# Performance work log

Hardware: AMD Instinct MI355X
Metric: run time of the kernel (lower is better)

## Reference

```python
import jax, jax.numpy as jnp
import numpy as np

INPUT_DIM = 1024
UNITS = 1024

def setup_inputs() -> dict:
    key = jax.random.key(0)
    ks = jax.random.split(key, 7)
    B, S = 4, 2048
    x = jax.random.normal(ks[0], (B, S, INPUT_DIM), dtype=jnp.float32)
    # nn.Linear weights stored as [out, in]; biases [out]
    scale = 1.0 / np.sqrt(INPUT_DIM)
    Wq = jax.random.uniform(ks[1], (UNITS, INPUT_DIM), jnp.float32, -scale, scale)
    bq = jax.random.uniform(ks[2], (UNITS,), jnp.float32, -scale, scale)
    Wk = jax.random.uniform(ks[3], (UNITS, INPUT_DIM), jnp.float32, -scale, scale)
    bk = jax.random.uniform(ks[4], (UNITS,), jnp.float32, -scale, scale)
    Wv = jax.random.uniform(ks[5], (UNITS, INPUT_DIM), jnp.float32, -scale, scale)
    bv = jax.random.uniform(ks[6], (UNITS,), jnp.float32, -scale, scale)
    return {"x": x, "Wq": Wq, "bq": bq, "Wk": Wk, "bk": bk, "Wv": Wv, "bv": bv}

def reference(x, Wq, bq, Wk, bk, Wv, bv):
    # Q/K/V projections: [B,S,D] @ [D,U]
    Q = jnp.einsum('bsd,ud->bsu', x, Wq) + bq
    K = jnp.einsum('bsd,ud->bsu', x, Wk) + bk
    V = jnp.einsum('bsd,ud->bsu', x, Wv) + bv
    scores = jnp.einsum('bqu,bku->bqk', Q, K) / jnp.sqrt(jnp.float32(UNITS))
    attn = jax.nn.softmax(scores, axis=-1)
    return jnp.einsum('bqk,bku->bqu', attn, V)
```

## Files before the change

### kernel.cpp

```cpp
#include <hip/hip_runtime.h>
#include <cstdint>
#include <cstddef>


typedef unsigned short ushort_t;
typedef __attribute__((ext_vector_type(8))) short short8;
typedef __attribute__((ext_vector_type(4))) float f32x4;

#define AS1 __attribute__((address_space(1)))
#define AS3 __attribute__((address_space(3)))

__device__ __forceinline__ ushort_t f2bf(float f) {
    unsigned int u = __float_as_uint(f);
    u += 0x7FFFu + ((u >> 16) & 1u);
    return (ushort_t)(u >> 16);
}
__device__ __forceinline__ float bf2f(ushort_t b) {
    return __uint_as_float(((unsigned)b) << 16);
}

__device__ __forceinline__ void async_ld16(const void* g, unsigned lds_off) {
    __builtin_amdgcn_global_load_lds((const AS1 void*)(uintptr_t)g,
                                     (AS3 void*)(uintptr_t)lds_off,
                                     16, 0, 0);
}

template <typename OT, int EPI, int NB, int BK>
__global__ __launch_bounds__(256, 2) void gemm_bt(
    const ushort_t* __restrict__ A, const ushort_t* __restrict__ B0,
    const ushort_t* __restrict__ B1,
    const float* __restrict__ bias0, const float* __restrict__ bias1,
    OT* __restrict__ C0, OT* __restrict__ C1,
    int K, int lda, int ldb, int ldc, float scale,
    long long aOffZ, long long bOffZ, long long cOffZ)
{
    constexpr int P     = BK / 8;
    constexpr int NCALL = BK / 16;
    constexpr int RPC   = 2048 / BK;

    __shared__ __align__(16) ushort_t As[128 * BK];
    __shared__ __align__(16) ushort_t Bs[NB][128 * BK];
    __shared__ float rs[128];

    const int tid  = threadIdx.x;
    const int wave = tid >> 6;
    const int lane = tid & 63;

    A  += (size_t)blockIdx.z * aOffZ;
    B0 += (size_t)blockIdx.z * bOffZ;
    if (NB == 2) B1 += (size_t)blockIdx.z * bOffZ;

    const int m0 = blockIdx.y * 128;
    const int n0 = blockIdx.x * 128;
    const int wm = (wave >> 1) * 64;
    const int wn = (wave & 1) * 64;

    const unsigned ldsA  = (unsigned)(uintptr_t)&As[0];
    const unsigned ldsB0 = (unsigned)(uintptr_t)&Bs[0][0];
    const unsigned ldsB1 = (NB == 2) ? (unsigned)(uintptr_t)&Bs[NB - 1][0] : 0;

    const int srow = wave * (RPC / 4) + lane / P;
    const int cd   = ((lane & (P - 1)) - srow) & (P - 1);
    const ushort_t* gA  = A  + (size_t)(m0 + srow) * lda + cd * 8;
    const ushort_t* gB0 = B0 + (size_t)(n0 + srow) * ldb + cd * 8;
    const ushort_t* gB1 = (NB == 2) ? B1 + (size_t)(n0 + srow) * ldb + cd * 8
                                    : nullptr;
    const unsigned lw = (wave << 10);

    const int frow = lane & 15;
    const int fg   = lane >> 4;

    f32x4 acc[NB][4][4] = {};
    float rsacc[4] = {0.f, 0.f, 0.f, 0.f};

    for (int k0 = 0; k0 < K; k0 += BK) {
        if (k0) __syncthreads();
#pragma unroll
        for (int c = 0; c < NCALL; ++c) {
            const size_t ro = (size_t)c * RPC;
            async_ld16(gA + ro * lda, ldsA + c * 4096 + lw);
            async_ld16(gB0 + ro * ldb, ldsB0 + c * 4096 + lw);
            if (NB == 2) async_ld16(gB1 + ro * ldb, ldsB1 + c * 4096 + lw);
        }
        gA += BK; gB0 += BK; if (NB == 2) gB1 += BK;
        __syncthreads();

#pragma unroll
        for (int t = 0; t < BK / 32; ++t) {
            const int pa = (((t << 2) + fg + frow) & (P - 1)) << 3;
            short8 af[4], bf[4];
#pragma unroll
            for (int i = 0; i < 4; ++i)
                af[i] = *(const short8*)&As[(wm + i * 16 + frow) * BK + pa];
            if (EPI == 4 && wn == 0) {
#pragma unroll
                for (int i = 0; i < 4; ++i)
#pragma unroll
                    for (int e = 0; e < 8; ++e)
                        rsacc[i] += bf2f((ushort_t)af[i][e]);
            }
#pragma unroll
            for (int j = 0; j < 4; ++j)
                bf[j] = *(const short8*)&Bs[0][(wn + j * 16 + frow) * BK + pa];
#pragma unroll
            for (int i = 0; i < 4; ++i)
#pragma unroll
                for (int j = 0; j < 4; ++j)
                    acc[0][i][j] = __builtin_amdgcn_mfma_f32_16x16x32_bf16(
                        af[i], bf[j], acc[0][i][j], 0, 0, 0);
            if (NB == 2) {
#pragma unroll
                for (int j = 0; j < 4; ++j)
                    bf[j] = *(const short8*)&Bs[NB - 1][(wn + j * 16 + frow) * BK + pa];
#pragma unroll
                for (int i = 0; i < 4; ++i)
#pragma unroll
                    for (int j = 0; j < 4; ++j)
                        acc[NB - 1][i][j] = __builtin_amdgcn_mfma_f32_16x16x32_bf16(
                            af[i], bf[j], acc[NB - 1][i][j], 0, 0, 0);
            }
        }
    }

    if (EPI == 4) {
        if (wn == 0) {
#pragma unroll
            for (int i = 0; i < 4; ++i) {
                float s = rsacc[i];
                s += __shfl_xor(s, 16, 64);
                s += __shfl_xor(s, 32, 64);
                rs[wm + i * 16 + frow] = s;
            }
        }
        __syncthreads();
    }

    const int r0 = (lane >> 4) << 2;
    const int c0 = lane & 15;
#pragma unroll
    for (int o = 0; o < NB; ++o) {
        OT* C = (o == 0) ? C0 : C1;
        C += (size_t)blockIdx.z * cOffZ;
        const float* bia = (o == 0) ? bias0 : bias1;
#pragma unroll
        for (int i = 0; i < 4; ++i) {
            float bm[4];
            if (EPI == 2) {
#pragma unroll
                for (int r = 0; r < 4; ++r)
                    bm[r] = bias0[m0 + wm + i * 16 + r0 + r];
            }
            if (EPI == 4) {
#pragma unroll
                for (int r = 0; r < 4; ++r)
                    bm[r] = 1.0f / rs[wm + i * 16 + r0 + r];
            }
#pragma unroll
            for (int j = 0; j < 4; ++j) {
                const int n = n0 + wn + j * 16 + c0;
                const float bn = (EPI == 1) ? bia[n] : 0.f;
#pragma unroll
                for (int r = 0; r < 4; ++r) {
                    const int m = m0 + wm + i * 16 + r0 + r;
                    float v = acc[o][i][j][r] * scale;
                    if (EPI == 1) v += bn;
                    if (EPI == 2) v += bm[r];
                    if (EPI == 3) v = __expf(v);
                    if (EPI == 4) v *= bm[r];
                    if constexpr (sizeof(OT) == 2)
                        C[(size_t)m * ldc + n] = f2bf(v);
                    else
                        C[(size_t)m * ldc + n] = v;
                }
            }
        }
    }
}

__global__ __launch_bounds__(256) void cvt_all(
    const float* __restrict__ x,  const float* __restrict__ wq,
    const float* __restrict__ wk, const float* __restrict__ wv,
    ushort_t* __restrict__ xb,  ushort_t* __restrict__ wqb,
    ushort_t* __restrict__ wkb, ushort_t* __restrict__ wvb)
{
    const int b = blockIdx.x;
    const float* src; ushort_t* dst; size_t base;
    if (b < 4096)      { src = x;  dst = xb;  base = (size_t)b * 2048; }
    else if (b < 4608) { src = wq; dst = wqb; base = (size_t)(b - 4096) * 2048; }
    else if (b < 5120) { src = wk; dst = wkb; base = (size_t)(b - 4608) * 2048; }
    else               { src = wv; dst = wvb; base = (size_t)(b - 5120) * 2048; }
    const size_t i = base + threadIdx.x * 8;
    const f32x4 a = *(const f32x4*)(src + i);
    const f32x4 c = *(const f32x4*)(src + i + 4);
    short8 o;
    o[0] = (short)f2bf(a[0]); o[1] = (short)f2bf(a[1]);
    o[2] = (short)f2bf(a[2]); o[3] = (short)f2bf(a[3]);
    o[4] = (short)f2bf(c[0]); o[5] = (short)f2bf(c[1]);
    o[6] = (short)f2bf(c[2]); o[7] = (short)f2bf(c[3]);
    *(short8*)(dst + i) = o;
}

extern "C" void kernel_launch(void* const* d_in, const int* in_sizes, int n_in,
                              void* d_out, int out_size, void* d_ws, size_t ws_size,
                              hipStream_t stream)
{
    const float* x  = (const float*)d_in[0];
    const float* Wq = (const float*)d_in[1];
    const float* bq = (const float*)d_in[2];
    const float* Wk = (const float*)d_in[3];
    const float* bk = (const float*)d_in[4];
    const float* Wv = (const float*)d_in[5];
    const float* bv = (const float*)d_in[6];
    float* out = (float*)d_out;

    char* ws = (char*)d_ws;
    const size_t MB = 1ull << 20;
    ushort_t* Xb  = (ushort_t*)(ws);
    ushort_t* Wqb = (ushort_t*)(ws + 16 * MB);
    ushort_t* Wkb = (ushort_t*)(ws + 18 * MB);
    ushort_t* Wvb = (ushort_t*)(ws + 20 * MB);
    ushort_t* Qb  = (ushort_t*)(ws + 32 * MB);
    ushort_t* Kb  = (ushort_t*)(ws + 48 * MB);
    ushort_t* Vt  = (ushort_t*)(ws + 64 * MB);
    ushort_t* Sc  = (ushort_t*)(ws);

    cvt_all<<<dim3(5632), dim3(256), 0, stream>>>(
        x, Wq, Wk, Wv, Xb, Wqb, Wkb, Wvb);

    gemm_bt<ushort_t, 1, 2, 64><<<dim3(8, 64, 1), dim3(256), 0, stream>>>(
        Xb, Wqb, Wkb, bq, bk, Qb, Kb, 1024, 1024, 1024, 1024, 1.0f, 0, 0, 0);

    gemm_bt<ushort_t, 2, 1, 64><<<dim3(64, 8, 1), dim3(256), 0, stream>>>(
        Wvb, Xb, nullptr, bv, nullptr, Vt, nullptr,
        1024, 1024, 1024, 8192, 1.0f, 0, 0, 0);

    gemm_bt<ushort_t, 3, 1, 64><<<dim3(16, 16, 4), dim3(256), 0, stream>>>(
        Qb, Kb, nullptr, nullptr, nullptr, Sc, nullptr,
        1024, 1024, 1024, 2048, 0.03125f,
        2048ll * 1024, 2048ll * 1024, 2048ll * 2048);

    gemm_bt<float, 4, 1, 64><<<dim3(8, 16, 4), dim3(256), 0, stream>>>(
        Sc, Vt, nullptr, nullptr, nullptr, out, nullptr,
        2048, 2048, 8192, 1024, 1.0f,
        2048ll * 2048, 2048ll, 2048ll * 1024);
}
```

Baseline: 249.9 us.

## Fuse QKV projections into one GEMM and swizzle block order for L2 locality

Merges the V projection into the Q/K projection kernel by loading a third weight tile per K step, reusing the shared X tile. V is written transposed with packed 4-element stores, which removes a separate launch and a second read of X. All GEMMs now use a 1D grid with a custom block-index remap that groups neighbouring tiles, apparently to line them up with the chip's XCD layout for cache reuse. The cost is more LDS and accumulator registers in the fused kernel (three B buffers, 48 accumulators), which may lower occupancy under launch_bounds(256,2).

```diff
diff --git a/kernel.cpp b/kernel.cpp
--- a/kernel.cpp
+++ b/kernel.cpp
@@ -4,6 +4,7 @@
 
 
 typedef unsigned short ushort_t;
+typedef __attribute__((ext_vector_type(4))) short short4v;
 typedef __attribute__((ext_vector_type(8))) short short8;
 typedef __attribute__((ext_vector_type(4))) float f32x4;
 
@@ -25,13 +26,14 @@
                                      16, 0, 0);
 }
 
-template <typename OT, int EPI, int NB, int BK>
+template <typename OT, int EPI, int NB, int BK, int SWZ>
 __global__ __launch_bounds__(256, 2) void gemm_bt(
     const ushort_t* __restrict__ A, const ushort_t* __restrict__ B0,
-    const ushort_t* __restrict__ B1,
+    const ushort_t* __restrict__ B1, const ushort_t* __restrict__ B2,
     const float* __restrict__ bias0, const float* __restrict__ bias1,
-    OT* __restrict__ C0, OT* __restrict__ C1,
-    int K, int lda, int ldb, int ldc, float scale,
+    const float* __restrict__ bias2,
+    OT* __restrict__ C0, OT* __restrict__ C1, ushort_t* __restrict__ C2,
+    int K, int lda, int ldb, int ldc, int ldc2, float scale,
     long long aOffZ, long long bOffZ, long long cOffZ)
 {
     constexpr int P     = BK / 8;
@@ -42,30 +44,44 @@
     __shared__ __align__(16) ushort_t Bs[NB][128 * BK];
     __shared__ float rs[128];
 
+    int bx, by, bz;
+    if (SWZ == 1) {
+        const int x = blockIdx.x & 7, s = blockIdx.x >> 3;
+        by = x * 8 + (s >> 3); bx = s & 7; bz = 0;
+    } else if (SWZ == 2) {
+        const int id = blockIdx.x; bz = id >> 8;
+        const int r = id & 255, x = r & 7, s = r >> 3;
+        by = (x >> 1) * 4 + (s & 3); bx = (x & 1) * 8 + (s >> 2);
+    } else {
+        const int id = blockIdx.x; bz = id >> 7;
+        const int r = id & 127, x = r & 7, s = r >> 3;
+        by = (x >> 1) * 4 + (s & 3); bx = (x & 1) * 4 + (s >> 2);
+    }
+
     const int tid  = threadIdx.x;
     const int wave = tid >> 6;
     const int lane = tid & 63;
 
-    A  += (size_t)blockIdx.z * aOffZ;
-    B0 += (size_t)blockIdx.z * bOffZ;
-    if (NB == 2) B1 += (size_t)blockIdx.z * bOffZ;
-
-    const int m0 = blockIdx.y * 128;
-    const int n0 = blockIdx.x * 128;
+    A  += (size_t)bz * aOffZ;
+    B0 += (size_t)bz * bOffZ;
+    if (NB >= 2) B1 += (size_t)bz * bOffZ;
+
+    const int m0 = by * 128;
+    const int n0 = bx * 128;
     const int wm = (wave >> 1) * 64;
     const int wn = (wave & 1) * 64;
 
     const unsigned ldsA  = (unsigned)(uintptr_t)&As[0];
     const unsigned ldsB0 = (unsigned)(uintptr_t)&Bs[0][0];
-    const unsigned ldsB1 = (NB == 2) ? (unsigned)(uintptr_t)&Bs[NB - 1][0] : 0;
 
     const int srow = wave * (RPC / 4) + lane / P;
     const int cd   = ((lane & (P - 1)) - srow) & (P - 1);
     const ushort_t* gA  = A  + (size_t)(m0 + srow) * lda + cd * 8;
     const ushort_t* gB0 = B0 + (size_t)(n0 + srow) * ldb + cd * 8;
-    const ushort_t* gB1 = (NB == 2) ? B1 + (size_t)(n0 + srow) * ldb + cd * 8
-                                    : nullptr;
+    const ushort_t* gB1 = (NB >= 2) ? B1 + (size_t)(n0 + srow) * ldb + cd * 8 : nullptr;
+    const ushort_t* gB2 = (NB >= 3) ? B2 + (size_t)(n0 + srow) * ldb + cd * 8 : nullptr;
     const unsigned lw = (wave << 10);
+    constexpr unsigned BSTEP = 128 * BK * 2;
 
     const int frow = lane & 15;
     const int fg   = lane >> 4;
@@ -80,9 +96,12 @@
             const size_t ro = (size_t)c * RPC;
             async_ld16(gA + ro * lda, ldsA + c * 4096 + lw);
             async_ld16(gB0 + ro * ldb, ldsB0 + c * 4096 + lw);
-            if (NB == 2) async_ld16(gB1 + ro * ldb, ldsB1 + c * 4096 + lw);
-        }
-        gA += BK; gB0 += BK; if (NB == 2) gB1 += BK;
+            if (NB >= 2) async_ld16(gB1 + ro * ldb, ldsB0 + BSTEP + c * 4096 + lw);
+            if (NB >= 3) async_ld16(gB2 + ro * ldb, ldsB0 + 2 * BSTEP + c * 4096 + lw);
+        }
+        gA += BK; gB0 += BK;
+        if (NB >= 2) gB1 += BK;
+        if (NB >= 3) gB2 += BK;
         __syncthreads();
 
 #pragma unroll
@@ -100,24 +119,16 @@
                         rsacc[i] += bf2f((ushort_t)af[i][e]);
             }
 #pragma unroll
-            for (int j = 0; j < 4; ++j)
-                bf[j] = *(const short8*)&Bs[0][(wn + j * 16 + frow) * BK + pa];
-#pragma unroll
-            for (int i = 0; i < 4; ++i)
+            for (int o = 0; o < NB; ++o) {
 #pragma unroll
                 for (int j = 0; j < 4; ++j)
-                    acc[0][i][j] = __builtin_amdgcn_mfma_f32_16x16x32_bf16(
-                        af[i], bf[j], acc[0][i][j], 0, 0, 0);
-            if (NB == 2) {
-#pragma unroll
-                for (int j = 0; j < 4; ++j)
-                    bf[j] = *(const short8*)&Bs[NB - 1][(wn + j * 16 + frow) * BK + pa];
+                    bf[j] = *(const short8*)&Bs[o][(wn + j * 16 + frow) * BK + pa];
 #pragma unroll
                 for (int i = 0; i < 4; ++i)
 #pragma unroll
                     for (int j = 0; j < 4; ++j)
-                        acc[NB - 1][i][j] = __builtin_amdgcn_mfma_f32_16x16x32_bf16(
-                            af[i], bf[j], acc[NB - 1][i][j], 0, 0, 0);
+                        acc[o][i][j] = __builtin_amdgcn_mfma_f32_16x16x32_bf16(
+                            af[i], bf[j], acc[o][i][j], 0, 0, 0);
             }
         }
     }
@@ -137,19 +148,15 @@
 
     const int r0 = (lane >> 4) << 2;
     const int c0 = lane & 15;
-#pragma unroll
-    for (int o = 0; o < NB; ++o) {
+    constexpr int NDIR = (NB == 3) ? 2 : NB;
+#pragma unroll
+    for (int o = 0; o < NDIR; ++o) {
         OT* C = (o == 0) ? C0 : C1;
-        C += (size_t)blockIdx.z * cOffZ;
+        C += (size_t)bz * cOffZ;
         const float* bia = (o == 0) ? bias0 : bias1;
 #pragma unroll
         for (int i = 0; i < 4; ++i) {
             float bm[4];
-            if (EPI == 2) {
-#pragma unroll
-                for (int r = 0; r < 4; ++r)
-                    bm[r] = bias0[m0 + wm + i * 16 + r0 + r];
-            }
             if (EPI == 4) {
 #pragma unroll
                 for (int r = 0; r < 4; ++r)
@@ -164,7 +171,6 @@
                     const int m = m0 + wm + i * 16 + r0 + r;
                     float v = acc[o][i][j][r] * scale;
                     if (EPI == 1) v += bn;
-                    if (EPI == 2) v += bm[r];
                     if (EPI == 3) v = __expf(v);
                     if (EPI == 4) v *= bm[r];
                     if constexpr (sizeof(OT) == 2)
@@ -172,6 +178,22 @@
                     else
                         C[(size_t)m * ldc + n] = v;
                 }
+            }
+        }
+    }
+    if (NB == 3) {
+#pragma unroll
+        for (int i = 0; i < 4; ++i) {
+#pragma unroll
+            for (int j = 0; j < 4; ++j) {
+                const int n = n0 + wn + j * 16 + c0;
+                const int m = m0 + wm + i * 16 + r0;
+                const float bn = bias2[n];
+                short4v pk;
+#pragma unroll
+                for (int r = 0; r < 4; ++r)
+                    pk[r] = (short)f2bf(acc[2][i][j][r] + bn);
+                *(short4v*)&C2[(size_t)n * ldc2 + m] = pk;
             }
         }
     }
@@ -227,20 +249,17 @@
     cvt_all<<<dim3(5632), dim3(256), 0, stream>>>(
         x, Wq, Wk, Wv, Xb, Wqb, Wkb, Wvb);
 
-    gemm_bt<ushort_t, 1, 2, 64><<<dim3(8, 64, 1), dim3(256), 0, stream>>>(
-        Xb, Wqb, Wkb, bq, bk, Qb, Kb, 1024, 1024, 1024, 1024, 1.0f, 0, 0, 0);
-
-    gemm_bt<ushort_t, 2, 1, 64><<<dim3(64, 8, 1), dim3(256), 0, stream>>>(
-        Wvb, Xb, nullptr, bv, nullptr, Vt, nullptr,
-        1024, 1024, 1024, 8192, 1.0f, 0, 0, 0);
-
-    gemm_bt<ushort_t, 3, 1, 64><<<dim3(16, 16, 4), dim3(256), 0, stream>>>(
-        Qb, Kb, nullptr, nullptr, nullptr, Sc, nullptr,
-        1024, 1024, 1024, 2048, 0.03125f,
+    gemm_bt<ushort_t, 1, 3, 64, 1><<<dim3(512), dim3(256), 0, stream>>>(
+        Xb, Wqb, Wkb, Wvb, bq, bk, bv, Qb, Kb, Vt,
+        1024, 1024, 1024, 1024, 8192, 1.0f, 0, 0, 0);
+
+    gemm_bt<ushort_t, 3, 1, 64, 2><<<dim3(1024), dim3(256), 0, stream>>>(
+        Qb, Kb, nullptr, nullptr, nullptr, nullptr, nullptr, Sc, nullptr, nullptr,
+        1024, 1024, 1024, 2048, 0, 0.03125f,
         2048ll * 1024, 2048ll * 1024, 2048ll * 2048);
 
-    gemm_bt<float, 4, 1, 64><<<dim3(8, 16, 4), dim3(256), 0, stream>>>(
-        Sc, Vt, nullptr, nullptr, nullptr, out, nullptr,
-        2048, 2048, 8192, 1024, 1.0f,
+    gemm_bt<float, 4, 1, 64, 3><<<dim3(512), dim3(256), 0, stream>>>(
+        Sc, Vt, nullptr, nullptr, nullptr, nullptr, nullptr, out, nullptr, nullptr,
+        2048, 2048, 8192, 1024, 0, 1.0f,
         2048ll * 2048, 2048ll, 2048ll * 1024);
 }
```

After: 300.2 us. 20.1% more time.

## Fuse Q, K and V projections into one 512-thread GEMM kernel

Applied to the files above, without the earlier changes.

Replaces the separate Q/K and V projection launches with a single qkv_gemm kernel. It uses 512 threads (8 waves) and keeps one X tile in LDS while it multiplies against three weight tiles, so X is loaded once for all three outputs and one launch is saved. V is written transposed using packed 4-element bf16 stores. The generic gemm_bt template is trimmed to a single-B path. The cost is a larger LDS footprint (64 KB) and 24 accumulator tiles per wave, which may lower occupancy.

```diff
diff --git a/kernel.cpp b/kernel.cpp
--- a/kernel.cpp
+++ b/kernel.cpp
@@ -4,6 +4,7 @@
 
 
 typedef unsigned short ushort_t;
+typedef __attribute__((ext_vector_type(4))) short short4v;
 typedef __attribute__((ext_vector_type(8))) short short8;
 typedef __attribute__((ext_vector_type(4))) float f32x4;
 
@@ -25,21 +26,130 @@
                                      16, 0, 0);
 }
 
-template <typename OT, int EPI, int NB, int BK>
+__global__ __launch_bounds__(512, 2) void qkv_gemm(
+    const ushort_t* __restrict__ X,
+    const ushort_t* __restrict__ W0, const ushort_t* __restrict__ W1,
+    const ushort_t* __restrict__ W2,
+    const float* __restrict__ b0, const float* __restrict__ b1,
+    const float* __restrict__ b2,
+    ushort_t* __restrict__ Q, ushort_t* __restrict__ Kout,
+    ushort_t* __restrict__ Vt)
+{
+    __shared__ __align__(16) ushort_t As[128 * 64];
+    __shared__ __align__(16) ushort_t Bs[3][128 * 64];
+
+    const int tid  = threadIdx.x;
+    const int wave = tid >> 6;
+    const int lane = tid & 63;
+
+    const int m0 = blockIdx.y * 128;
+    const int n0 = blockIdx.x * 128;
+    const int wm = (wave >> 2) * 64;
+    const int wn = (wave & 3) * 32;
+
+    const unsigned ldsA = (unsigned)(uintptr_t)&As[0];
+    const unsigned ldsB = (unsigned)(uintptr_t)&Bs[0][0];
+    constexpr unsigned BSTEP = 128 * 64 * 2;
+
+    const int srow = (wave << 3) + (lane >> 3);
+    const int cd   = ((lane & 7) - (lane >> 3)) & 7;
+    const ushort_t* gX  = X  + (size_t)(m0 + srow) * 1024 + cd * 8;
+    const ushort_t* gW0 = W0 + (size_t)(n0 + srow) * 1024 + cd * 8;
+    const ushort_t* gW1 = W1 + (size_t)(n0 + srow) * 1024 + cd * 8;
+    const ushort_t* gW2 = W2 + (size_t)(n0 + srow) * 1024 + cd * 8;
+    const unsigned lw = (wave << 10);
+
+    const int frow = lane & 15;
+    const int fg   = lane >> 4;
+
+    f32x4 acc[3][4][2] = {};
+
+    for (int k0 = 0; k0 < 1024; k0 += 64) {
+        if (k0) __syncthreads();
+#pragma unroll
+        for (int c = 0; c < 2; ++c) {
+            const size_t ro = (size_t)c * 64;
+            async_ld16(gX  + ro * 1024, ldsA + c * 8192 + lw);
+            async_ld16(gW0 + ro * 1024, ldsB + 0 * BSTEP + c * 8192 + lw);
+            async_ld16(gW1 + ro * 1024, ldsB + 1 * BSTEP + c * 8192 + lw);
+            async_ld16(gW2 + ro * 1024, ldsB + 2 * BSTEP + c * 8192 + lw);
+        }
+        gX += 64; gW0 += 64; gW1 += 64; gW2 += 64;
+        __syncthreads();
+
+#pragma unroll
+        for (int t = 0; t < 2; ++t) {
+            const int ck = (t << 2) + fg;
+            short8 af[4], bf[2];
+#pragma unroll
+            for (int i = 0; i < 4; ++i) {
+                const int row = wm + i * 16 + frow;
+                af[i] = *(const short8*)&As[row * 64 + (((ck + row) & 7) << 3)];
+            }
+#pragma unroll
+            for (int o = 0; o < 3; ++o) {
+#pragma unroll
+                for (int j = 0; j < 2; ++j) {
+                    const int row = wn + j * 16 + frow;
+                    bf[j] = *(const short8*)&Bs[o][row * 64 + (((ck + row) & 7) << 3)];
+                }
+#pragma unroll
+                for (int i = 0; i < 4; ++i)
+#pragma unroll
+                    for (int j = 0; j < 2; ++j)
+                        acc[o][i][j] = __builtin_amdgcn_mfma_f32_16x16x32_bf16(
+                            af[i], bf[j], acc[o][i][j], 0, 0, 0);
+            }
+        }
+    }
+
+    const int r0 = (lane >> 4) << 2;
+    const int c0 = lane & 15;
+#pragma unroll
+    for (int o = 0; o < 2; ++o) {
+        ushort_t* C = (o == 0) ? Q : Kout;
+        const float* bia = (o == 0) ? b0 : b1;
+#pragma unroll
+        for (int i = 0; i < 4; ++i) {
+#pragma unroll
+            for (int j = 0; j < 2; ++j) {
+                const int n = n0 + wn + j * 16 + c0;
+                const float bn = bia[n];
+#pragma unroll
+                for (int r = 0; r < 4; ++r) {
+                    const int m = m0 + wm + i * 16 + r0 + r;
+                    C[(size_t)m * 1024 + n] = f2bf(acc[o][i][j][r] + bn);
+                }
+            }
+        }
+    }
+#pragma unroll
+    for (int i = 0; i < 4; ++i) {
+#pragma unroll
+        for (int j = 0; j < 2; ++j) {
+            const int n = n0 + wn + j * 16 + c0;
+            const int m = m0 + wm + i * 16 + r0;
+            const float bn = b2[n];
+            short4v pk;
+#pragma unroll
+            for (int r = 0; r < 4; ++r)
+                pk[r] = (short)f2bf(acc[2][i][j][r] + bn);
+            *(short4v*)&Vt[(size_t)n * 8192 + m] = pk;
+        }
+    }
+}
+
+template <typename OT, int EPI>
 __global__ __launch_bounds__(256, 2) void gemm_bt(
     const ushort_t* __restrict__ A, const ushort_t* __restrict__ B0,
-    const ushort_t* __restrict__ B1,
-    const float* __restrict__ bias0, const float* __restrict__ bias1,
-    OT* __restrict__ C0, OT* __restrict__ C1,
+    OT* __restrict__ C0,
     int K, int lda, int ldb, int ldc, float scale,
     long long aOffZ, long long bOffZ, long long cOffZ)
 {
-    constexpr int P     = BK / 8;
-    constexpr int NCALL = BK / 16;
-    constexpr int RPC   = 2048 / BK;
+    constexpr int BK = 64, P = 8, NCALL = 4, RPC = 32;
 
     __shared__ __align__(16) ushort_t As[128 * BK];
-    __shared__ __align__(16) ushort_t Bs[NB][128 * BK];
+    __shared__ __align__(16) ushort_t Bs[128 * BK];
     __shared__ float rs[128];
 
     const int tid  = threadIdx.x;
@@ -48,29 +158,25 @@
 
     A  += (size_t)blockIdx.z * aOffZ;
     B0 += (size_t)blockIdx.z * bOffZ;
-    if (NB == 2) B1 += (size_t)blockIdx.z * bOffZ;
 
     const int m0 = blockIdx.y * 128;
     const int n0 = blockIdx.x * 128;
     const int wm = (wave >> 1) * 64;
     const int wn = (wave & 1) * 64;
 
-    const unsigned ldsA  = (unsigned)(uintptr_t)&As[0];
-    const unsigned ldsB0 = (unsigned)(uintptr_t)&Bs[0][0];
-    const unsigned ldsB1 = (NB == 2) ? (unsigned)(uintptr_t)&Bs[NB - 1][0] : 0;
+    const unsigned ldsA = (unsigned)(uintptr_t)&As[0];
+    const unsigned ldsB = (unsigned)(uintptr_t)&Bs[0];
 
     const int srow = wave * (RPC / 4) + lane / P;
     const int cd   = ((lane & (P - 1)) - srow) & (P - 1);
     const ushort_t* gA  = A  + (size_t)(m0 + srow) * lda + cd * 8;
     const ushort_t* gB0 = B0 + (size_t)(n0 + srow) * ldb + cd * 8;
-    const ushort_t* gB1 = (NB == 2) ? B1 + (size_t)(n0 + srow) * ldb + cd * 8
-                                    : nullptr;
     const unsigned lw = (wave << 10);
 
     const int frow = lane & 15;
     const int fg   = lane >> 4;
 
-    f32x4 acc[NB][4][4] = {};
+    f32x4 acc[4][4] = {};
     float rsacc[4] = {0.f, 0.f, 0.f, 0.f};
 
     for (int k0 = 0; k0 < K; k0 += BK) {
@@ -79,14 +185,13 @@
         for (int c = 0; c < NCALL; ++c) {
             const size_t ro = (size_t)c * RPC;
             async_ld16(gA + ro * lda, ldsA + c * 4096 + lw);
-            async_ld16(gB0 + ro * ldb, ldsB0 + c * 4096 + lw);
-            if (NB == 2) async_ld16(gB1 + ro * ldb, ldsB1 + c * 4096 + lw);
-        }
-        gA += BK; gB0 += BK; if (NB == 2) gB1 += BK;
+            async_ld16(gB0 + ro * ldb, ldsB + c * 4096 + lw);
+        }
+        gA += BK; gB0 += BK;
         __syncthreads();
 
 #pragma unroll
-        for (int t = 0; t < BK / 32; ++t) {
+        for (int t = 0; t < 2; ++t) {
             const int pa = (((t << 2) + fg + frow) & (P - 1)) << 3;
             short8 af[4], bf[4];
 #pragma unroll
@@ -101,24 +206,13 @@
             }
 #pragma unroll
             for (int j = 0; j < 4; ++j)
-                bf[j] = *(const short8*)&Bs[0][(wn + j * 16 + frow) * BK + pa];
+                bf[j] = *(const short8*)&Bs[(wn + j * 16 + frow) * BK + pa];
 #pragma unroll
             for (int i = 0; i < 4; ++i)
 #pragma unroll
                 for (int j = 0; j < 4; ++j)
-                    acc[0][i][j] = __builtin_amdgcn_mfma_f32_16x16x32_bf16(
-                        af[i], bf[j], acc[0][i][j], 0, 0, 0);
-            if (NB == 2) {
-#pragma unroll
-                for (int j = 0; j < 4; ++j)
-                    bf[j] = *(const short8*)&Bs[NB - 1][(wn + j * 16 + frow) * BK + pa];
-#pragma unroll
-                for (int i = 0; i < 4; ++i)
-#pragma unroll
-                    for (int j = 0; j < 4; ++j)
-                        acc[NB - 1][i][j] = __builtin_amdgcn_mfma_f32_16x16x32_bf16(
-                            af[i], bf[j], acc[NB - 1][i][j], 0, 0, 0);
-            }
+                    acc[i][j] = __builtin_amdgcn_mfma_f32_16x16x32_bf16(
+                        af[i], bf[j], acc[i][j], 0, 0, 0);
         }
     }
 
@@ -137,41 +231,28 @@
 
     const int r0 = (lane >> 4) << 2;
     const int c0 = lane & 15;
-#pragma unroll
-    for (int o = 0; o < NB; ++o) {
-        OT* C = (o == 0) ? C0 : C1;
-        C += (size_t)blockIdx.z * cOffZ;
-        const float* bia = (o == 0) ? bias0 : bias1;
-#pragma unroll
-        for (int i = 0; i < 4; ++i) {
-            float bm[4];
-            if (EPI == 2) {
-#pragma unroll
-                for (int r = 0; r < 4; ++r)
-                    bm[r] = bias0[m0 + wm + i * 16 + r0 + r];
-            }
-            if (EPI == 4) {
-#pragma unroll
-                for (int r = 0; r < 4; ++r)
-                    bm[r] = 1.0f / rs[wm + i * 16 + r0 + r];
-            }
-#pragma unroll
-            for (int j = 0; j < 4; ++j) {
-                const int n = n0 + wn + j * 16 + c0;
-                const float bn = (EPI == 1) ? bia[n] : 0.f;
-#pragma unroll
-                for (int r = 0; r < 4; ++r) {
-                    const int m = m0 + wm + i * 16 + r0 + r;
-                    float v = acc[o][i][j][r] * scale;
-                    if (EPI == 1) v += bn;
-                    if (EPI == 2) v += bm[r];
-                    if (EPI == 3) v = __expf(v);
-                    if (EPI == 4) v *= bm[r];
-                    if constexpr (sizeof(OT) == 2)
-                        C[(size_t)m * ldc + n] = f2bf(v);
-                    else
-                        C[(size_t)m * ldc + n] = v;
-                }
+    OT* C = C0 + (size_t)blockIdx.z * cOffZ;
+#pragma unroll
+    for (int i = 0; i < 4; ++i) {
+        float bm[4];
+        if (EPI == 4) {
+#pragma unroll
+            for (int r = 0; r < 4; ++r)
+                bm[r] = 1.0f / rs[wm + i * 16 + r0 + r];
+        }
+#pragma unroll
+        for (int j = 0; j < 4; ++j) {
+            const int n = n0 + wn + j * 16 + c0;
+#pragma unroll
+            for (int r = 0; r < 4; ++r) {
+                const int m = m0 + wm + i * 16 + r0 + r;
+                float v = acc[i][j][r] * scale;
+                if (EPI == 3) v = __expf(v);
+                if (EPI == 4) v *= bm[r];
+                if constexpr (sizeof(OT) == 2)
+                    C[(size_t)m * ldc + n] = f2bf(v);
+                else
+                    C[(size_t)m * ldc + n] = v;
             }
         }
     }
@@ -227,20 +308,14 @@
     cvt_all<<<dim3(5632), dim3(256), 0, stream>>>(
         x, Wq, Wk, Wv, Xb, Wqb, Wkb, Wvb);
 
-    gemm_bt<ushort_t, 1, 2, 64><<<dim3(8, 64, 1), dim3(256), 0, stream>>>(
-        Xb, Wqb, Wkb, bq, bk, Qb, Kb, 1024, 1024, 1024, 1024, 1.0f, 0, 0, 0);
-
-    gemm_bt<ushort_t, 2, 1, 64><<<dim3(64, 8, 1), dim3(256), 0, stream>>>(
-        Wvb, Xb, nullptr, bv, nullptr, Vt, nullptr,
-        1024, 1024, 1024, 8192, 1.0f, 0, 0, 0);
-
-    gemm_bt<ushort_t, 3, 1, 64><<<dim3(16, 16, 4), dim3(256), 0, stream>>>(
-        Qb, Kb, nullptr, nullptr, nullptr, Sc, nullptr,
-        1024, 1024, 1024, 2048, 0.03125f,
+    qkv_gemm<<<dim3(8, 64), dim3(512), 0, stream>>>(
+        Xb, Wqb, Wkb, Wvb, bq, bk, bv, Qb, Kb, Vt);
+
+    gemm_bt<ushort_t, 3><<<dim3(16, 16, 4), dim3(256), 0, stream>>>(
+        Qb, Kb, Sc, 1024, 1024, 1024, 2048, 0.03125f,
         2048ll * 1024, 2048ll * 1024, 2048ll * 2048);
 
-    gemm_bt<float, 4, 1, 64><<<dim3(8, 16, 4), dim3(256), 0, stream>>>(
-        Sc, Vt, nullptr, nullptr, nullptr, out, nullptr,
-        2048, 2048, 8192, 1024, 1.0f,
+    gemm_bt<float, 4><<<dim3(8, 16, 4), dim3(256), 0, stream>>>(
+        Sc, Vt, out, 2048, 2048, 8192, 1024, 1.0f,
         2048ll * 2048, 2048ll, 2048ll * 1024);
 }
```

After: 267.9 us. 7.2% more time.
